# Optimization experiments

Measured on AMD Instinct MI355X. Metric: run time of the kernel, lower is better.

Reference implementation:

```python
import jax, jax.numpy as jnp
import numpy as np

N_NODES = 50000
N_EDGES = 800000
HIDDEN = 128
EDGE_DIM = 16
N_HEADS = 8
HEAD_DIM = HIDDEN // N_HEADS
SCALE = 1.0 / np.sqrt(HEAD_DIM).astype(np.float32)
LN_EPS = 1e-5


def setup_inputs() -> dict:
    key = jax.random.key(0)
    ks = jax.random.split(key, 24)
    s = 0.02

    def w(k, shape):
        return jax.random.normal(k, shape, dtype=jnp.float32) * s

    inp = {
        "node_features": jax.random.normal(ks[0], (N_NODES, HIDDEN), dtype=jnp.float32),
        "edge_index": jax.random.randint(ks[1], (2, N_EDGES), 0, N_NODES, dtype=jnp.int32),
        "edge_features": jax.random.normal(ks[2], (N_EDGES, EDGE_DIM), dtype=jnp.float32),
        # projections stored as [in, out] (y = x @ W + b)
        "Wq": w(ks[3], (HIDDEN, HIDDEN)), "bq": jnp.zeros((HIDDEN,), jnp.float32),
        "Wk": w(ks[4], (HIDDEN, HIDDEN)), "bk": jnp.zeros((HIDDEN,), jnp.float32),
        "Wv": w(ks[5], (HIDDEN, HIDDEN)), "bv": jnp.zeros((HIDDEN,), jnp.float32),
        "Wb1": w(ks[6], (EDGE_DIM, N_HEADS)), "bb1": jnp.zeros((N_HEADS,), jnp.float32),
        "Wb2": w(ks[7], (N_HEADS, N_HEADS)), "bb2": jnp.zeros((N_HEADS,), jnp.float32),
        "Wo": w(ks[8], (HIDDEN, HIDDEN)), "bo": jnp.zeros((HIDDEN,), jnp.float32),
        "Wf1": w(ks[9], (HIDDEN, 2 * HIDDEN)), "bf1": jnp.zeros((2 * HIDDEN,), jnp.float32),
        "Wf2": w(ks[10], (2 * HIDDEN, HIDDEN)), "bf2": jnp.zeros((HIDDEN,), jnp.float32),
        "g1": jnp.ones((HIDDEN,), jnp.float32), "be1": jnp.zeros((HIDDEN,), jnp.float32),
        "g2": jnp.ones((HIDDEN,), jnp.float32), "be2": jnp.zeros((HIDDEN,), jnp.float32),
    }
    return inp


def _layer_norm(x, gamma, beta):
    mu = jnp.mean(x, axis=-1, keepdims=True)
    var = jnp.mean(jnp.square(x - mu), axis=-1, keepdims=True)
    return (x - mu) * jax.lax.rsqrt(var + LN_EPS) * gamma + beta


def reference(node_features, edge_index, edge_features,
              Wq, bq, Wk, bk, Wv, bv, Wb1, bb1, Wb2, bb2,
              Wo, bo, Wf1, bf1, Wf2, bf2, g1, be1, g2, be2):
    n_nodes = node_features.shape[0]
    src, dst = edge_index[0], edge_index[1]

    q = (node_features @ Wq + bq).reshape(n_nodes, N_HEADS, HEAD_DIM)
    k = (node_features @ Wk + bk).reshape(n_nodes, N_HEADS, HEAD_DIM)
    v = (node_features @ Wv + bv).reshape(n_nodes, N_HEADS, HEAD_DIM)

    # per-edge attention logits [E, H]
    edge_bias = jax.nn.silu(edge_features @ Wb1 + bb1) @ Wb2 + bb2
    logits = jnp.sum(q[dst] * k[src], axis=-1) * SCALE + edge_bias

    # segment softmax over edges sharing the same dst node
    max_s = jax.ops.segment_max(logits, dst, num_segments=n_nodes)
    exp_s = jnp.exp(logits - max_s[dst])
    norm = jax.ops.segment_sum(exp_s, dst, num_segments=n_nodes)
    attn = exp_s / jnp.clip(norm[dst], 1e-12)

    # weighted aggregation [N, H, D] -> [N, hidden]
    weighted = attn[:, :, None] * v[src]
    aggregated = jax.ops.segment_sum(weighted, dst, num_segments=n_nodes)
    aggregated = aggregated.reshape(n_nodes, HIDDEN)

    x = _layer_norm(node_features + (aggregated @ Wo + bo), g1, be1)
    ffn = jax.nn.silu(x @ Wf1 + bf1) @ Wf2 + bf2
    return _layer_norm(x + ffn, g2, be2)
```

## Files before the change

kernel.cpp:

```cpp
#include <hip/hip_runtime.h>
#include <hip/hip_bf16.h>
#include <math.h>

#define HIDDEN 128
#define EDGE_DIM 16
#define N_HEADS 8
#define QK_SCALE 0.25f
#define LN_EPS 1e-5f
#define EB_SCALE 256.0f
#define EB_INV (1.0f / 256.0f)

using bf16x8 = __attribute__((ext_vector_type(8))) short;
using f32x4 = __attribute__((ext_vector_type(4))) float;
using f32x4v = __attribute__((ext_vector_type(4))) float;
using f32x2 = __attribute__((ext_vector_type(2))) float;
using i32x4 = __attribute__((ext_vector_type(4))) int;
typedef __hip_bfloat16 bf16;

__device__ __forceinline__ float b2f(short u) {
  union { unsigned int i; float f; } c;
  c.i = ((unsigned int)(unsigned short)u) << 16;
  return c.f;
}
__device__ __forceinline__ short f2b(float f) {
  bf16 h = __float2bfloat16(f);
  union { bf16 b; short s; } c;
  c.b = h;
  return c.s;
}
__device__ __forceinline__ unsigned char f2fp8(float f) {
  int pk = __builtin_amdgcn_cvt_pk_fp8_f32(f, f, 0, false);
  return (unsigned char)(pk & 0xff);
}

__global__ __launch_bounds__(256) void conv_weights_kernel(
    const float* __restrict__ Wq, const float* __restrict__ Wk, const float* __restrict__ Wv,
    const float* __restrict__ bq, const float* __restrict__ bk, const float* __restrict__ bv,
    const float* __restrict__ Wo, const float* __restrict__ Wf1, const float* __restrict__ Wf2,
    bf16* __restrict__ Wqkv_t, bf16* __restrict__ Wo_t, bf16* __restrict__ Wf1_t,
    bf16* __restrict__ Wf2_t, float* __restrict__ bqkv) {
  int i = blockIdx.x * 256 + threadIdx.x;
  if (i < 49152) {
    int n = i >> 7, k = i & 127;
    const float* W = (n < 128) ? Wq : ((n < 256) ? Wk : Wv);
    int nn = n & 127;
    Wqkv_t[i] = __float2bfloat16(W[k * 128 + nn]);
  } else if (i < 65536) {
    int j = i - 49152;
    int n = j >> 7, k = j & 127;
    Wo_t[j] = __float2bfloat16(Wo[k * 128 + n]);
  } else if (i < 98304) {
    int j = i - 65536;
    int n = j >> 7, k = j & 127;
    Wf1_t[j] = __float2bfloat16(Wf1[k * 256 + n]);
  } else if (i < 131072) {
    int j = i - 98304;
    int n = j >> 8, k = j & 255;
    Wf2_t[j] = __float2bfloat16(Wf2[k * 128 + n]);
  }
  if (i < 384) bqkv[i] = (i < 128) ? bq[i] : ((i < 256) ? bk[i - 128] : bv[i - 256]);
}

template <int K, int EPI, int OUTBF, int AF32>
__global__ __launch_bounds__(256) void mfma_gemm_kernel(
    const void* __restrict__ Ap, const bf16* __restrict__ Wt,
    const float* __restrict__ bias, void* __restrict__ Cout, int M, int Nc) {
  const int tid = threadIdx.x;
  const int w = tid >> 6, l = tid & 63;
  const int wr = w >> 1, wc = w & 1;
  const int lr = l & 15, lk = l >> 4;
  const int bm = blockIdx.y * 64;
  const int bn = blockIdx.x * 128 + wc * 64;

  f32x4 acc[2][4] = {};
  const int arow0 = bm + wr * 32 + lr;

  for (int k0 = 0; k0 < K; k0 += 128) {
    bf16x8 bfr[4][4];
#pragma unroll
    for (int fn = 0; fn < 4; ++fn) {
      const bf16* wp = Wt + (size_t)(bn + fn * 16 + lr) * K + k0 + lk * 8;
#pragma unroll
      for (int ks = 0; ks < 4; ++ks) bfr[fn][ks] = *(const bf16x8*)(wp + ks * 32);
    }
    bf16x8 afr[2][4];
#pragma unroll
    for (int fr = 0; fr < 2; ++fr) {
      int row = arow0 + fr * 16;
      if (row >= M) row = M - 1;
      if (AF32) {
        const float* ap = (const float*)Ap + (size_t)row * K + k0 + lk * 8;
#pragma unroll
        for (int ks = 0; ks < 4; ++ks) {
          float4 x = *(const float4*)(ap + ks * 32);
          float4 y = *(const float4*)(ap + ks * 32 + 4);
          bf16x8 t;
          t[0] = f2b(x.x); t[1] = f2b(x.y); t[2] = f2b(x.z); t[3] = f2b(x.w);
          t[4] = f2b(y.x); t[5] = f2b(y.y); t[6] = f2b(y.z); t[7] = f2b(y.w);
          afr[fr][ks] = t;
        }
      } else {
        const bf16* ap = (const bf16*)Ap + (size_t)row * K + k0 + lk * 8;
#pragma unroll
        for (int ks = 0; ks < 4; ++ks) afr[fr][ks] = *(const bf16x8*)(ap + ks * 32);
      }
    }
#pragma unroll
    for (int ks = 0; ks < 4; ++ks)
#pragma unroll
      for (int fr = 0; fr < 2; ++fr)
#pragma unroll
        for (int fn = 0; fn < 4; ++fn)
          acc[fr][fn] = __builtin_amdgcn_mfma_f32_16x16x32_bf16(afr[fr][ks], bfr[fn][ks],
                                                                acc[fr][fn], 0, 0, 0);
  }

#pragma unroll
  for (int fn = 0; fn < 4; ++fn) {
    const int col = bn + fn * 16 + lr;
    const float bv = bias[col];
#pragma unroll
    for (int fr = 0; fr < 2; ++fr) {
      const int rbase = bm + wr * 32 + fr * 16 + lk * 4;
#pragma unroll
      for (int r = 0; r < 4; ++r) {
        int row = rbase + r;
        if (row < M) {
          float o = acc[fr][fn][r] + bv;
          if (EPI == 1) o = o / (1.f + __expf(-o));
          if (OUTBF)
            ((bf16*)Cout)[(size_t)row * Nc + col] = __float2bfloat16(o);
          else
            ((float*)Cout)[(size_t)row * Nc + col] = o;
        }
      }
    }
  }
}

__global__ __launch_bounds__(256) void mfma_gemm_qkv_kernel(
    const float* __restrict__ A, const bf16* __restrict__ Wt,
    const float* __restrict__ bias, bf16* __restrict__ qb,
    unsigned char* __restrict__ kv8, int M) {
  __shared__ __align__(16) char lds[64 * 272];
  const int tid = threadIdx.x;
  const int w = tid >> 6, l = tid & 63;
  const int wr = w >> 1, wc = w & 1;
  const int lr = l & 15, lk = l >> 4;
  const int bm = blockIdx.y * 64;
  const int bn = blockIdx.x * 128 + wc * 64;

  f32x4 acc[2][4] = {};
  const int arow0 = bm + wr * 32 + lr;

  {
    bf16x8 bfr[4][4];
#pragma unroll
    for (int fn = 0; fn < 4; ++fn) {
      const bf16* wp = Wt + (size_t)(bn + fn * 16 + lr) * 128 + lk * 8;
#pragma unroll
      for (int ks = 0; ks < 4; ++ks) bfr[fn][ks] = *(const bf16x8*)(wp + ks * 32);
    }
    bf16x8 afr[2][4];
#pragma unroll
    for (int fr = 0; fr < 2; ++fr) {
      int row = arow0 + fr * 16;
      if (row >= M) row = M - 1;
      const float* ap = A + (size_t)row * 128 + lk * 8;
#pragma unroll
      for (int ks = 0; ks < 4; ++ks) {
        float4 x = *(const float4*)(ap + ks * 32);
        float4 y = *(const float4*)(ap + ks * 32 + 4);
        bf16x8 t;
        t[0] = f2b(x.x); t[1] = f2b(x.y); t[2] = f2b(x.z); t[3] = f2b(x.w);
        t[4] = f2b(y.x); t[5] = f2b(y.y); t[6] = f2b(y.z); t[7] = f2b(y.w);
        afr[fr][ks] = t;
      }
    }
#pragma unroll
    for (int ks = 0; ks < 4; ++ks)
#pragma unroll
      for (int fr = 0; fr < 2; ++fr)
#pragma unroll
        for (int fn = 0; fn < 4; ++fn)
          acc[fr][fn] = __builtin_amdgcn_mfma_f32_16x16x32_bf16(afr[fr][ks], bfr[fn][ks],
                                                                acc[fr][fn], 0, 0, 0);
  }

  const bool isQ = (blockIdx.x == 0);
  if (isQ) {
    short* sq = (short*)lds;
#pragma unroll
    for (int fn = 0; fn < 4; ++fn) {
      const int col = wc * 64 + fn * 16 + lr;
      const float bv = bias[bn + fn * 16 + lr];
#pragma unroll
      for (int fr = 0; fr < 2; ++fr) {
#pragma unroll
        for (int r = 0; r < 4; ++r) {
          int rl = wr * 32 + fr * 16 + lk * 4 + r;
          sq[rl * 136 + col] = f2b(acc[fr][fn][r] + bv);
        }
      }
    }
  } else {
    unsigned char* s8 = (unsigned char*)lds;
#pragma unroll
    for (int fn = 0; fn < 4; ++fn) {
      const int col = wc * 64 + fn * 16 + lr;
      const float bv = bias[bn + fn * 16 + lr];
#pragma unroll
      for (int fr = 0; fr < 2; ++fr) {
#pragma unroll
        for (int r = 0; r < 4; ++r) {
          int rl = wr * 32 + fr * 16 + lk * 4 + r;
          s8[rl * 144 + col] = f2fp8(acc[fr][fn][r] + bv);
        }
      }
    }
  }
  __syncthreads();

  const int row = tid >> 2, seg = tid & 3;
  const int grow = bm + row;
  if (grow < M) {
    if (isQ) {
      const int4* src = (const int4*)(lds + row * 272 + seg * 64);
      int4* dst = (int4*)(qb + (size_t)grow * 128 + seg * 32);
      dst[0] = src[0];
      dst[1] = src[1];
      dst[2] = src[2];
      dst[3] = src[3];
    } else {
      const int4* src = (const int4*)(lds + row * 144 + seg * 32);
      int4* dst = (int4*)(kv8 + (size_t)grow * 256 + (blockIdx.x == 1 ? 0 : 128) + seg * 32);
      dst[0] = src[0];
      dst[1] = src[1];
    }
  }
}

template <int K>
__global__ __launch_bounds__(256) void mfma_gemm_ln_kernel(
    const bf16* __restrict__ A, const bf16* __restrict__ Wt,
    const float* __restrict__ bias, const float* __restrict__ R,
    const float* __restrict__ gam, const float* __restrict__ bet,
    float* __restrict__ y, bf16* __restrict__ yb, int M) {
  const int tid = threadIdx.x;
  const int w = tid >> 6, l = tid & 63;
  const int wr = w >> 1, wc = w & 1;
  const int lr = l & 15, lk = l >> 4;
  const int bm = blockIdx.x * 64;
  const int bn = wc * 64;

  f32x4 acc[2][4] = {};
  const int arow0 = bm + wr * 32 + lr;

  for (int k0 = 0; k0 < K; k0 += 128) {
    bf16x8 bfr[4][4];
#pragma unroll
    for (int fn = 0; fn < 4; ++fn) {
      const bf16* wp = Wt + (size_t)(bn + fn * 16 + lr) * K + k0 + lk * 8;
#pragma unroll
      for (int ks = 0; ks < 4; ++ks) bfr[fn][ks] = *(const bf16x8*)(wp + ks * 32);
    }
    bf16x8 afr[2][4];
#pragma unroll
    for (int fr = 0; fr < 2; ++fr) {
      int row = arow0 + fr * 16;
      if (row >= M) row = M - 1;
      const bf16* ap = A + (size_t)row * K + k0 + lk * 8;
#pragma unroll
      for (int ks = 0; ks < 4; ++ks) afr[fr][ks] = *(const bf16x8*)(ap + ks * 32);
    }
#pragma unroll
    for (int ks = 0; ks < 4; ++ks)
#pragma unroll
      for (int fr = 0; fr < 2; ++fr)
#pragma unroll
        for (int fn = 0; fn < 4; ++fn)
          acc[fr][fn] = __builtin_amdgcn_mfma_f32_16x16x32_bf16(afr[fr][ks], bfr[fn][ks],
                                                                acc[fr][fn], 0, 0, 0);
  }

  float bv[4], gv[4], ev[4];
#pragma unroll
  for (int fn = 0; fn < 4; ++fn) {
    int col = bn + fn * 16 + lr;
    bv[fn] = bias[col];
    gv[fn] = gam[col];
    ev[fn] = bet[col];
  }
  float ps[2][4], psq[2][4];
#pragma unroll
  for (int fr = 0; fr < 2; ++fr) {
#pragma unroll
    for (int r = 0; r < 4; ++r) {
      int row = bm + wr * 32 + fr * 16 + lk * 4 + r;
      int rrow = (row < M) ? row : (M - 1);
      float s = 0.f, sq = 0.f;
#pragma unroll
      for (int fn = 0; fn < 4; ++fn) {
        int col = bn + fn * 16 + lr;
        float o = acc[fr][fn][r] + bv[fn] + R[(size_t)rrow * HIDDEN + col];
        acc[fr][fn][r] = o;
        s += o;
        sq += o * o;
      }
      ps[fr][r] = s;
      psq[fr][r] = sq;
    }
  }
#pragma unroll
  for (int off = 1; off < 16; off <<= 1) {
#pragma unroll
    for (int fr = 0; fr < 2; ++fr)
#pragma unroll
      for (int r = 0; r < 4; ++r) {
        ps[fr][r] += __shfl_xor(ps[fr][r], off, 64);
        psq[fr][r] += __shfl_xor(psq[fr][r], off, 64);
      }
  }
  __shared__ float s_sum[2][64], s_sq[2][64];
  if (lr == 0) {
#pragma unroll
    for (int fr = 0; fr < 2; ++fr)
#pragma unroll
      for (int r = 0; r < 4; ++r) {
        int rl = wr * 32 + fr * 16 + lk * 4 + r;
        s_sum[wc][rl] = ps[fr][r];
        s_sq[wc][rl] = psq[fr][r];
      }
  }
  __syncthreads();
#pragma unroll
  for (int fr = 0; fr < 2; ++fr) {
#pragma unroll
    for (int r = 0; r < 4; ++r) {
      int rl = wr * 32 + fr * 16 + lk * 4 + r;
      int row = bm + rl;
      float tot = s_sum[0][rl] + s_sum[1][rl];
      float tsq = s_sq[0][rl] + s_sq[1][rl];
      float mean = tot * (1.f / 128.f);
      float var = tsq * (1.f / 128.f) - mean * mean;
      float rstd = rsqrtf(var + LN_EPS);
      if (row < M) {
#pragma unroll
        for (int fn = 0; fn < 4; ++fn) {
          int col = bn + fn * 16 + lr;
          float val = (acc[fr][fn][r] - mean) * rstd * gv[fn] + ev[fn];
          if (y) y[(size_t)row * HIDDEN + col] = val;
          if (yb) yb[(size_t)row * HIDDEN + col] = __float2bfloat16(val);
        }
      }
    }
  }
}

__global__ void hist_kernel(const int* __restrict__ dst, int* __restrict__ counts, int E) {
  int e = blockIdx.x * blockDim.x + threadIdx.x;
  if (e < E) atomicAdd(&counts[dst[e]], 1);
}

__device__ __forceinline__ int wave_incl_scan(int x, int lane) {
  int incl = x;
#pragma unroll
  for (int off = 1; off < 64; off <<= 1) {
    int y = __shfl_up(incl, off, 64);
    if (lane >= off) incl += y;
  }
  return incl;
}

__global__ __launch_bounds__(256) void scan_block_kernel(const int* __restrict__ counts,
                                                         int* __restrict__ offs,
                                                         int* __restrict__ btot, int N) {
  __shared__ int s4[4];
  int tid = threadIdx.x;
  int i = blockIdx.x * 256 + tid;
  int lane = tid & 63, wv = tid >> 6;
  int x = (i < N) ? counts[i] : 0;
  int incl = wave_incl_scan(x, lane);
  if (lane == 63) s4[wv] = incl;
  __syncthreads();
  if (tid == 0) {
    int s = 0;
#pragma unroll
    for (int j = 0; j < 4; ++j) { int t = s4[j]; s4[j] = s; s += t; }
    btot[blockIdx.x] = s;
  }
  __syncthreads();
  if (i < N) offs[i] = s4[wv] + incl - x;
}

__global__ __launch_bounds__(256) void scan_tot_kernel(int* __restrict__ btot, int nb) {
  __shared__ int s4[4];
  __shared__ int carry;
  int tid = threadIdx.x;
  int lane = tid & 63, wv = tid >> 6;
  if (tid == 0) carry = 0;
  __syncthreads();
  for (int c0 = 0; c0 < nb; c0 += 256) {
    int i = c0 + tid;
    int x = (i < nb) ? btot[i] : 0;
    int incl = wave_incl_scan(x, lane);
    if (lane == 63) s4[wv] = incl;
    __syncthreads();
    if (tid == 0) {
      int s = 0;
#pragma unroll
      for (int j = 0; j < 4; ++j) { int t = s4[j]; s4[j] = s; s += t; }
    }
    __syncthreads();
    int base = carry + s4[wv];
    if (i < nb) btot[i] = base + incl - x;
    __syncthreads();
    if (tid == 255) carry = base + incl;
    __syncthreads();
  }
}

__global__ __launch_bounds__(256) void scan_add_kernel(int* __restrict__ offs,
                                                       const int* __restrict__ btot,
                                                       int N, int E) {
  int i = blockIdx.x * 256 + threadIdx.x;
  if (i < N) offs[i] += btot[blockIdx.x];
  if (i == 0) offs[N] = E;
}

__global__ __launch_bounds__(256) void scatter_mlp_kernel(
    const int* __restrict__ dst, const int* __restrict__ src,
    const float* __restrict__ ef, const float* __restrict__ Wb1,
    const float* __restrict__ bb1, const float* __restrict__ Wb2,
    const float* __restrict__ bb2, const int* __restrict__ offs,
    int* __restrict__ cursor, i32x4* __restrict__ es16, int E) {
  __shared__ float w1[128], w2[64], b1[8], b2[8];
  int tid = threadIdx.x;
  if (tid < 128) w1[tid] = Wb1[tid];
  else if (tid < 192) w2[tid - 128] = Wb2[tid - 128];
  else if (tid < 200) b1[tid - 192] = bb1[tid - 192];
  else if (tid < 208) b2[tid - 200] = bb2[tid - 200];
  __syncthreads();

  int e = blockIdx.x * 256 + tid;
  if (e >= E) return;

  const f32x4v* p4 = (const f32x4v*)(ef + (size_t)e * 16);
  f32x4v f0 = __builtin_nontemporal_load(p4 + 0);
  f32x4v f1 = __builtin_nontemporal_load(p4 + 1);
  f32x4v f2 = __builtin_nontemporal_load(p4 + 2);
  f32x4v f3 = __builtin_nontemporal_load(p4 + 3);
  float x[16] = {f0[0], f0[1], f0[2], f0[3], f1[0], f1[1], f1[2], f1[3],
                 f2[0], f2[1], f2[2], f2[3], f3[0], f3[1], f3[2], f3[3]};

  float h[8];
#pragma unroll
  for (int j = 0; j < 8; ++j) h[j] = b1[j];
#pragma unroll
  for (int i = 0; i < 16; ++i) {
    float xi = x[i];
#pragma unroll
    for (int j = 0; j < 8; ++j) h[j] = fmaf(xi, w1[i * 8 + j], h[j]);
  }
#pragma unroll
  for (int j = 0; j < 8; ++j) h[j] = h[j] / (1.f + __expf(-h[j]));

  float o[8];
#pragma unroll
  for (int j = 0; j < 8; ++j) o[j] = b2[j];
#pragma unroll
  for (int jj = 0; jj < 8; ++jj) {
    float hj = h[jj];
#pragma unroll
    for (int j = 0; j < 8; ++j) o[j] = fmaf(hj, w2[jj * 8 + j], o[j]);
  }

  int lo = __builtin_amdgcn_cvt_pk_fp8_f32(o[0] * EB_SCALE, o[1] * EB_SCALE, 0, false);
  lo = __builtin_amdgcn_cvt_pk_fp8_f32(o[2] * EB_SCALE, o[3] * EB_SCALE, lo, true);
  int hi = __builtin_amdgcn_cvt_pk_fp8_f32(o[4] * EB_SCALE, o[5] * EB_SCALE, 0, false);
  hi = __builtin_amdgcn_cvt_pk_fp8_f32(o[6] * EB_SCALE, o[7] * EB_SCALE, hi, true);

  int d = dst[e];
  int p = offs[d] + atomicAdd(&cursor[d], 1);
  i32x4 rec;
  rec[0] = src[e]; rec[1] = lo; rec[2] = hi; rec[3] = 0;
  __builtin_nontemporal_store(rec, es16 + p);
}

__global__ __launch_bounds__(256) void node_attn_kernel(
    const bf16* __restrict__ qb, const unsigned char* __restrict__ kv8,
    const i32x4* __restrict__ es16, const int* __restrict__ offs,
    bf16* __restrict__ agg, int Nn) {
  int n = blockIdx.x * 4 + (threadIdx.x >> 6);
  if (n >= Nn) return;
  int l = threadIdx.x & 63;
  int g = l >> 3;
  int il = l & 7;

  int s0 = offs[n], s1 = offs[n + 1];
  bf16* orow = agg + (size_t)n * HIDDEN + il * 16;
  if (s0 >= s1) {
    if (g == 0) {
      bf16x8 z = {};
      *(bf16x8*)(orow) = z;
      *(bf16x8*)(orow + 8) = z;
    }
    return;
  }

  const bf16* qrow = qb + (size_t)n * 128 + il * 16;
  bf16x8 qa = *(const bf16x8*)(qrow);
  bf16x8 qb8 = *(const bf16x8*)(qrow + 8);
  float qf[16];
#pragma unroll
  for (int j = 0; j < 8; ++j) {
    qf[j] = b2f(qa[j]) * QK_SCALE;
    qf[8 + j] = b2f(qb8[j]) * QK_SCALE;
  }

  float lsum = 0.f;
  float acc[16] = {};
  const int ebshift = (il & 2) << 3;

  for (int p0 = s0; p0 < s1; p0 += 8) {
    int p = p0 + g;
    bool valid = p < s1;
    int pc = valid ? p : s1 - 1;
    i32x4 rec = es16[pc];
    int cs = rec[0];
    unsigned ebw = (unsigned)((il < 4) ? rec[1] : rec[2]);
    f32x2 ebp = __builtin_amdgcn_cvt_pk_f32_fp8(ebw >> ebshift, false);
    float ebv = ((il & 1) ? ebp[1] : ebp[0]) * EB_INV;

    const unsigned char* kvrow = kv8 + (size_t)cs * 256 + il * 16;
    i32x4 kw = *(const i32x4*)(kvrow);
    i32x4 vw = *(const i32x4*)(kvrow + 128);

    float prod = 0.f;
#pragma unroll
    for (int w2 = 0; w2 < 4; ++w2) {
      f32x2 lo = __builtin_amdgcn_cvt_pk_f32_fp8(kw[w2], false);
      f32x2 hi = __builtin_amdgcn_cvt_pk_f32_fp8(kw[w2], true);
      prod = fmaf(qf[w2 * 4 + 0], lo[0], prod);
      prod = fmaf(qf[w2 * 4 + 1], lo[1], prod);
      prod = fmaf(qf[w2 * 4 + 2], hi[0], prod);
      prod = fmaf(qf[w2 * 4 + 3], hi[1], prod);
    }
    float pe = valid ? __expf(prod + ebv) : 0.f;
    lsum += pe;
#pragma unroll
    for (int w2 = 0; w2 < 4; ++w2) {
      f32x2 lo = __builtin_amdgcn_cvt_pk_f32_fp8(vw[w2], false);
      f32x2 hi = __builtin_amdgcn_cvt_pk_f32_fp8(vw[w2], true);
      acc[w2 * 4 + 0] = fmaf(pe, lo[0], acc[w2 * 4 + 0]);
      acc[w2 * 4 + 1] = fmaf(pe, lo[1], acc[w2 * 4 + 1]);
      acc[w2 * 4 + 2] = fmaf(pe, hi[0], acc[w2 * 4 + 2]);
      acc[w2 * 4 + 3] = fmaf(pe, hi[1], acc[w2 * 4 + 3]);
    }
  }

#pragma unroll
  for (int off = 8; off < 64; off <<= 1) {
    lsum += __shfl_xor(lsum, off, 64);
#pragma unroll
    for (int j = 0; j < 16; ++j) acc[j] += __shfl_xor(acc[j], off, 64);
  }

  if (g == 0) {
    float inv = (lsum > 0.f) ? 1.f / lsum : 0.f;
    bf16x8 o0, o1;
#pragma unroll
    for (int j = 0; j < 8; ++j) {
      o0[j] = f2b(acc[j] * inv);
      o1[j] = f2b(acc[8 + j] * inv);
    }
    *(bf16x8*)(orow) = o0;
    *(bf16x8*)(orow + 8) = o1;
  }
}

extern "C" void kernel_launch(void* const* d_in, const int* in_sizes, int n_in,
                              void* d_out, int out_size, void* d_ws, size_t ws_size,
                              hipStream_t stream) {
  const float* nf = (const float*)d_in[0];
  const int* ei = (const int*)d_in[1];
  const float* ef = (const float*)d_in[2];
  const float* Wq = (const float*)d_in[3];
  const float* bq = (const float*)d_in[4];
  const float* Wk = (const float*)d_in[5];
  const float* bk_ = (const float*)d_in[6];
  const float* Wv = (const float*)d_in[7];
  const float* bv = (const float*)d_in[8];
  const float* Wb1 = (const float*)d_in[9];
  const float* bb1 = (const float*)d_in[10];
  const float* Wb2 = (const float*)d_in[11];
  const float* bb2 = (const float*)d_in[12];
  const float* Wo = (const float*)d_in[13];
  const float* bo = (const float*)d_in[14];
  const float* Wf1 = (const float*)d_in[15];
  const float* bf1 = (const float*)d_in[16];
  const float* Wf2 = (const float*)d_in[17];
  const float* bf2 = (const float*)d_in[18];
  const float* g1 = (const float*)d_in[19];
  const float* be1 = (const float*)d_in[20];
  const float* g2 = (const float*)d_in[21];
  const float* be2 = (const float*)d_in[22];

  const int N = in_sizes[0] / HIDDEN;
  const int E = in_sizes[2] / EDGE_DIM;
  const int* srcA = ei;
  const int* dstA = ei + E;

  char* base = (char*)d_ws;
  size_t off = 0;
  auto alloc = [&](size_t bytes) {
    off = (off + 255) & ~(size_t)255;
    char* p = base + off;
    off += bytes;
    return p;
  };

  size_t qb_bytes = (size_t)N * 128 * 2;
  size_t kv_bytes = (size_t)N * 256;
  size_t hb_bytes = (size_t)N * 256 * 2;
  char* regB = alloc(hb_bytes > qb_bytes + kv_bytes ? hb_bytes : qb_bytes + kv_bytes);
  bf16* qb = (bf16*)regB;
  unsigned char* kv8 = (unsigned char*)(regB + qb_bytes);
  bf16* hbuf = (bf16*)regB;
  bf16* agg = (bf16*)alloc((size_t)N * HIDDEN * 2);
  float* x1 = (float*)alloc((size_t)N * HIDDEN * 4);
  bf16* x1b = (bf16*)alloc((size_t)N * HIDDEN * 2);
  i32x4* es16 = (i32x4*)alloc((size_t)E * 16);
  int* counts = (int*)alloc((size_t)N * 8);
  int* cursor = counts + N;
  int* offs = (int*)alloc((size_t)(N + 1) * 4);
  const int nb = (N + 255) / 256;
  int* btot = (int*)alloc((size_t)nb * 4);
  bf16* Wqkv_t = (bf16*)alloc(384 * 128 * 2);
  bf16* Wo_t = (bf16*)alloc(128 * 128 * 2);
  bf16* Wf1_t = (bf16*)alloc(256 * 128 * 2);
  bf16* Wf2_t = (bf16*)alloc(128 * 256 * 2);
  float* bqkv = (float*)alloc(384 * 4);

  float* outp = (float*)d_out;
  const int mb64 = (N + 63) / 64;
  const int eblocks = (E + 255) / 256;

  conv_weights_kernel<<<512, 256, 0, stream>>>(Wq, Wk, Wv, bq, bk_, bv, Wo, Wf1, Wf2,
                                               Wqkv_t, Wo_t, Wf1_t, Wf2_t, bqkv);

  mfma_gemm_qkv_kernel<<<dim3(3, mb64), 256, 0, stream>>>(nf, Wqkv_t, bqkv, qb, kv8, N);

  hipMemsetAsync(counts, 0, (size_t)N * 8, stream);
  hist_kernel<<<eblocks, 256, 0, stream>>>(dstA, counts, E);
  scan_block_kernel<<<nb, 256, 0, stream>>>(counts, offs, btot, N);
  scan_tot_kernel<<<1, 256, 0, stream>>>(btot, nb);
  scan_add_kernel<<<nb, 256, 0, stream>>>(offs, btot, N, E);
  scatter_mlp_kernel<<<eblocks, 256, 0, stream>>>(dstA, srcA, ef, Wb1, bb1, Wb2, bb2,
                                                  offs, cursor, es16, E);

  node_attn_kernel<<<(N + 3) / 4, 256, 0, stream>>>(qb, kv8, es16, offs, agg, N);

  mfma_gemm_ln_kernel<128><<<mb64, 256, 0, stream>>>(agg, Wo_t, bo, nf, g1, be1, x1, x1b, N);

  mfma_gemm_kernel<128, 1, 1, 0><<<dim3(2, mb64), 256, 0, stream>>>(
      x1b, Wf1_t, bf1, hbuf, N, 256);

  mfma_gemm_ln_kernel<256><<<mb64, 256, 0, stream>>>(hbuf, Wf2_t, bf2, x1, g2, be2,
                                                     outp, nullptr, N);
}
```

Measured before the change: 272.2 us.

## Two-pass bucketed scatter of edges into CSR to localize writes

Replaces the direct random scatter of edge records into CSR order with two passes. The first pass bins edges by dst>>8 into 196 coarse buckets using block-local counters in shared memory. The second pass places each bucket's records into their final CSR slots, one bucket per block. The aim is to turn scattered 16-byte writes and global atomics into more local ones, at the cost of an extra E*16-byte buffer round trip and two extra launches.

```diff
diff --git a/kernel.cpp b/kernel.cpp
--- a/kernel.cpp
+++ b/kernel.cpp
@@ -357,9 +357,21 @@
   }
 }
 
-__global__ void hist_kernel(const int* __restrict__ dst, int* __restrict__ counts, int E) {
-  int e = blockIdx.x * blockDim.x + threadIdx.x;
-  if (e < E) atomicAdd(&counts[dst[e]], 1);
+__global__ __launch_bounds__(256) void hist_kernel(const int* __restrict__ dst,
+                                                   int* __restrict__ counts,
+                                                   int* __restrict__ bcounts, int E) {
+  __shared__ int lb[256];
+  int tid = threadIdx.x;
+  lb[tid] = 0;
+  __syncthreads();
+  int e = blockIdx.x * 256 + tid;
+  if (e < E) {
+    int d = dst[e];
+    atomicAdd(&counts[d], 1);
+    atomicAdd(&lb[d >> 8], 1);
+  }
+  __syncthreads();
+  if (lb[tid]) atomicAdd(&bcounts[tid], lb[tid]);
 }
 
 __device__ __forceinline__ int wave_incl_scan(int x, int lane) {
@@ -428,63 +440,105 @@
   if (i == 0) offs[N] = E;
 }
 
+__global__ __launch_bounds__(256) void bscan_kernel(const int* __restrict__ bcounts,
+                                                    int* __restrict__ boffs) {
+  __shared__ int s4[4];
+  int tid = threadIdx.x, lane = tid & 63, wv = tid >> 6;
+  int x = bcounts[tid];
+  int incl = wave_incl_scan(x, lane);
+  if (lane == 63) s4[wv] = incl;
+  __syncthreads();
+  if (tid == 0) {
+    int s = 0;
+#pragma unroll
+    for (int j = 0; j < 4; ++j) { int t = s4[j]; s4[j] = s; s += t; }
+  }
+  __syncthreads();
+  boffs[tid] = s4[wv] + incl - x;
+  if (tid == 255) boffs[256] = s4[3] + incl;
+}
+
 __global__ __launch_bounds__(256) void scatter_mlp_kernel(
     const int* __restrict__ dst, const int* __restrict__ src,
     const float* __restrict__ ef, const float* __restrict__ Wb1,
     const float* __restrict__ bb1, const float* __restrict__ Wb2,
-    const float* __restrict__ bb2, const int* __restrict__ offs,
-    int* __restrict__ cursor, i32x4* __restrict__ es16, int E) {
+    const float* __restrict__ bb2, const int* __restrict__ boffs,
+    int* __restrict__ bcursor, i32x4* __restrict__ ebuf, int E) {
   __shared__ float w1[128], w2[64], b1[8], b2[8];
+  __shared__ int lcnt[256], lbase[256];
   int tid = threadIdx.x;
   if (tid < 128) w1[tid] = Wb1[tid];
   else if (tid < 192) w2[tid - 128] = Wb2[tid - 128];
   else if (tid < 200) b1[tid - 192] = bb1[tid - 192];
   else if (tid < 208) b2[tid - 200] = bb2[tid - 200];
+  lcnt[tid] = 0;
   __syncthreads();
 
   int e = blockIdx.x * 256 + tid;
-  if (e >= E) return;
-
-  const f32x4v* p4 = (const f32x4v*)(ef + (size_t)e * 16);
-  f32x4v f0 = __builtin_nontemporal_load(p4 + 0);
-  f32x4v f1 = __builtin_nontemporal_load(p4 + 1);
-  f32x4v f2 = __builtin_nontemporal_load(p4 + 2);
-  f32x4v f3 = __builtin_nontemporal_load(p4 + 3);
-  float x[16] = {f0[0], f0[1], f0[2], f0[3], f1[0], f1[1], f1[2], f1[3],
-                 f2[0], f2[1], f2[2], f2[3], f3[0], f3[1], f3[2], f3[3]};
-
-  float h[8];
-#pragma unroll
-  for (int j = 0; j < 8; ++j) h[j] = b1[j];
-#pragma unroll
-  for (int i = 0; i < 16; ++i) {
-    float xi = x[i];
-#pragma unroll
-    for (int j = 0; j < 8; ++j) h[j] = fmaf(xi, w1[i * 8 + j], h[j]);
-  }
-#pragma unroll
-  for (int j = 0; j < 8; ++j) h[j] = h[j] / (1.f + __expf(-h[j]));
-
-  float o[8];
-#pragma unroll
-  for (int j = 0; j < 8; ++j) o[j] = b2[j];
-#pragma unroll
-  for (int jj = 0; jj < 8; ++jj) {
-    float hj = h[jj];
-#pragma unroll
-    for (int j = 0; j < 8; ++j) o[j] = fmaf(hj, w2[jj * 8 + j], o[j]);
-  }
-
-  int lo = __builtin_amdgcn_cvt_pk_fp8_f32(o[0] * EB_SCALE, o[1] * EB_SCALE, 0, false);
-  lo = __builtin_amdgcn_cvt_pk_fp8_f32(o[2] * EB_SCALE, o[3] * EB_SCALE, lo, true);
-  int hi = __builtin_amdgcn_cvt_pk_fp8_f32(o[4] * EB_SCALE, o[5] * EB_SCALE, 0, false);
-  hi = __builtin_amdgcn_cvt_pk_fp8_f32(o[6] * EB_SCALE, o[7] * EB_SCALE, hi, true);
-
-  int d = dst[e];
-  int p = offs[d] + atomicAdd(&cursor[d], 1);
-  i32x4 rec;
-  rec[0] = src[e]; rec[1] = lo; rec[2] = hi; rec[3] = 0;
-  __builtin_nontemporal_store(rec, es16 + p);
+  bool val = e < E;
+  int b = 0, myidx = 0;
+  i32x4 rec = {};
+  if (val) {
+    const f32x4v* p4 = (const f32x4v*)(ef + (size_t)e * 16);
+    f32x4v f0 = __builtin_nontemporal_load(p4 + 0);
+    f32x4v f1 = __builtin_nontemporal_load(p4 + 1);
+    f32x4v f2 = __builtin_nontemporal_load(p4 + 2);
+    f32x4v f3 = __builtin_nontemporal_load(p4 + 3);
+    float x[16] = {f0[0], f0[1], f0[2], f0[3], f1[0], f1[1], f1[2], f1[3],
+                   f2[0], f2[1], f2[2], f2[3], f3[0], f3[1], f3[2], f3[3]};
+
+    float h[8];
+#pragma unroll
+    for (int j = 0; j < 8; ++j) h[j] = b1[j];
+#pragma unroll
+    for (int i = 0; i < 16; ++i) {
+      float xi = x[i];
+#pragma unroll
+      for (int j = 0; j < 8; ++j) h[j] = fmaf(xi, w1[i * 8 + j], h[j]);
+    }
+#pragma unroll
+    for (int j = 0; j < 8; ++j) h[j] = h[j] / (1.f + __expf(-h[j]));
+
+    float o[8];
+#pragma unroll
+    for (int j = 0; j < 8; ++j) o[j] = b2[j];
+#pragma unroll
+    for (int jj = 0; jj < 8; ++jj) {
+      float hj = h[jj];
+#pragma unroll
+      for (int j = 0; j < 8; ++j) o[j] = fmaf(hj, w2[jj * 8 + j], o[j]);
+    }
+
+    int lo = __builtin_amdgcn_cvt_pk_fp8_f32(o[0] * EB_SCALE, o[1] * EB_SCALE, 0, false);
+    lo = __builtin_amdgcn_cvt_pk_fp8_f32(o[2] * EB_SCALE, o[3] * EB_SCALE, lo, true);
+    int hi = __builtin_amdgcn_cvt_pk_fp8_f32(o[4] * EB_SCALE, o[5] * EB_SCALE, 0, false);
+    hi = __builtin_amdgcn_cvt_pk_fp8_f32(o[6] * EB_SCALE, o[7] * EB_SCALE, hi, true);
+
+    int d = dst[e];
+    b = d >> 8;
+    rec[0] = src[e]; rec[1] = lo; rec[2] = hi; rec[3] = d;
+    myidx = atomicAdd(&lcnt[b], 1);
+  }
+  __syncthreads();
+  if (lcnt[tid] > 0) lbase[tid] = atomicAdd(&bcursor[tid], lcnt[tid]);
+  __syncthreads();
+  if (val) {
+    ebuf[(size_t)boffs[b] + lbase[b] + myidx] = rec;
+  }
+}
+
+__global__ __launch_bounds__(256) void csr_place_kernel(
+    const i32x4* __restrict__ ebuf, const int* __restrict__ boffs,
+    const int* __restrict__ offs, int* __restrict__ cursor,
+    i32x4* __restrict__ es16, int E) {
+  int b = blockIdx.x;
+  int st = boffs[b], en = boffs[b + 1];
+  for (int i = st + threadIdx.x; i < en; i += 256) {
+    i32x4 rec = ebuf[i];
+    int d = rec[3];
+    int p = offs[d] + atomicAdd(&cursor[d], 1);
+    es16[p] = rec;
+  }
 }
 
 __global__ __launch_bounds__(256) void node_attn_kernel(
@@ -631,9 +685,13 @@
   float* x1 = (float*)alloc((size_t)N * HIDDEN * 4);
   bf16* x1b = (bf16*)alloc((size_t)N * HIDDEN * 2);
   i32x4* es16 = (i32x4*)alloc((size_t)E * 16);
-  int* counts = (int*)alloc((size_t)N * 8);
+  i32x4* ebuf = (i32x4*)alloc((size_t)E * 16);
+  int* counts = (int*)alloc(((size_t)N * 2 + 512) * 4);
   int* cursor = counts + N;
+  int* bcounts = counts + 2 * N;
+  int* bcursor = bcounts + 256;
   int* offs = (int*)alloc((size_t)(N + 1) * 4);
+  int* boffs = (int*)alloc(257 * 4);
   const int nb = (N + 255) / 256;
   int* btot = (int*)alloc((size_t)nb * 4);
   bf16* Wqkv_t = (bf16*)alloc(384 * 128 * 2);
@@ -651,13 +709,16 @@
 
   mfma_gemm_qkv_kernel<<<dim3(3, mb64), 256, 0, stream>>>(nf, Wqkv_t, bqkv, qb, kv8, N);
 
-  hipMemsetAsync(counts, 0, (size_t)N * 8, stream);
-  hist_kernel<<<eblocks, 256, 0, stream>>>(dstA, counts, E);
+  hipMemsetAsync(counts, 0, ((size_t)N * 2 + 512) * 4, stream);
+  hist_kernel<<<eblocks, 256, 0, stream>>>(dstA, counts, bcounts, E);
   scan_block_kernel<<<nb, 256, 0, stream>>>(counts, offs, btot, N);
   scan_tot_kernel<<<1, 256, 0, stream>>>(btot, nb);
   scan_add_kernel<<<nb, 256, 0, stream>>>(offs, btot, N, E);
+  bscan_kernel<<<1, 256, 0, stream>>>(bcounts, boffs);
+
   scatter_mlp_kernel<<<eblocks, 256, 0, stream>>>(dstA, srcA, ef, Wb1, bb1, Wb2, bb2,
-                                                  offs, cursor, es16, E);
+                                                  boffs, bcursor, ebuf, E);
+  csr_place_kernel<<<256, 256, 0, stream>>>(ebuf, boffs, offs, cursor, es16, E);
 
   node_attn_kernel<<<(N + 3) / 4, 256, 0, stream>>>(qb, kv8, es16, offs, agg, N);
 
```

After: 361.7 us. 32.9% more time.
